# Performance work log

Measured on AMD Instinct MI355X. Metric: run time of the kernel, lower is better.

## Reference

```python
import jax, jax.numpy as jnp
import numpy as np

TEMPERATURE = 0.07
NEG_INF = -1e9  # fp16-safe large negative for masking


def setup_inputs() -> dict:
    key = jax.random.key(0)
    k1, k2 = jax.random.split(key)
    N, D = 4096, 1024
    logits1 = jax.random.normal(k1, (N, D), dtype=jnp.float32)
    logits2 = jax.random.normal(k2, (N, D), dtype=jnp.float32)
    return {"logits1": logits1, "logits2": logits2}


def reference(logits1, logits2):
    # L2-normalize each view along feature dim
    z1 = logits1 / jnp.linalg.norm(logits1, axis=1, keepdims=True)
    z2 = logits2 / jnp.linalg.norm(logits2, axis=1, keepdims=True)
    z = jnp.concatenate([z1, z2], axis=0)  # [2N, D]
    N2 = z.shape[0]
    N = N2 // 2
    sim = jnp.matmul(z, z.T) / TEMPERATURE  # [2N, 2N]
    # positive pair index: i <-> i+N (mod 2N)
    pos_idx = jnp.concatenate([jnp.arange(N) + N, jnp.arange(N)])
    pos_vals = sim[jnp.arange(N2), pos_idx]  # [2N]
    # CE over row = [pos, negs(excl self & pos)] with label 0 is equivalent to
    # -pos + logsumexp over all columns except the diagonal (pos counted once).
    diag_mask = jnp.eye(N2, dtype=bool)
    sim_masked = jnp.where(diag_mask, NEG_INF, sim)
    lse = jax.nn.logsumexp(sim_masked, axis=1)  # [2N]
    loss = jnp.mean(lse - pos_vals)
    return loss
```

## Files before the change

### kernel.cpp

```cpp
#include <hip/hip_runtime.h>
#include <hip/hip_bf16.h>


#define NPAIR 4096
#define NROWS 8192
#define DIM   1024
#define NOFF  496
#define NKT   16
#define INV_T 14.285714285714286f

typedef __attribute__((ext_vector_type(4))) float f32x4;
typedef __attribute__((ext_vector_type(2))) long  i64x2;

#define GLOAD_LDS16(g, l)                                              \
  __builtin_amdgcn_global_load_lds(                                    \
      (const __attribute__((address_space(1))) void*)(g),              \
      (__attribute__((address_space(3))) void*)(l), 16, 0, 0)

#define MFMA_FP8(A, B, C)                                              \
  __builtin_amdgcn_mfma_f32_16x16x32_fp8_fp8((long)(A), (long)(B), (C), 0, 0, 0)

#define WAIT_VM0() asm volatile("s_waitcnt vmcnt(0)" ::: "memory")
#define BARRIER()  { __builtin_amdgcn_s_barrier();                     \
                     __builtin_amdgcn_sched_barrier(0); }

__global__ __launch_bounds__(256) void normalize_kernel(
    const float* __restrict__ l1, const float* __restrict__ l2,
    unsigned char* __restrict__ Z, float* __restrict__ pos,
    float* __restrict__ rowsum) {
  const int i = blockIdx.x;
  const int t = threadIdx.x;
  if (t < 2) rowsum[i * 2 + t] = 0.f;
  const float4 a = ((const float4*)(l1 + (size_t)i * DIM))[t];
  const float4 b = ((const float4*)(l2 + (size_t)i * DIM))[t];
  float s1 = a.x*a.x + a.y*a.y + a.z*a.z + a.w*a.w;
  float s2 = b.x*b.x + b.y*b.y + b.z*b.z + b.w*b.w;
  float d  = a.x*b.x + a.y*b.y + a.z*b.z + a.w*b.w;

  #pragma unroll
  for (int off = 32; off; off >>= 1) {
    s1 += __shfl_down(s1, off);
    s2 += __shfl_down(s2, off);
    d  += __shfl_down(d,  off);
  }
  __shared__ float red[3][4];
  __shared__ float fin[3];
  const int wave = t >> 6, lane = t & 63;
  if (lane == 0) { red[0][wave] = s1; red[1][wave] = s2; red[2][wave] = d; }
  __syncthreads();
  if (t == 0) {
    float S1 = red[0][0] + red[0][1] + red[0][2] + red[0][3];
    float S2 = red[1][0] + red[1][1] + red[1][2] + red[1][3];
    float DD = red[2][0] + red[2][1] + red[2][2] + red[2][3];
    float r1 = rsqrtf(S1), r2 = rsqrtf(S2);
    fin[0] = r1; fin[1] = r2;
    pos[i] = DD * r1 * r2 * INV_T;
  }
  __syncthreads();
  const float r1 = fin[0], r2 = fin[1];
  int pa = __builtin_amdgcn_cvt_pk_fp8_f32(a.x * r1, a.y * r1, 0, false);
  pa     = __builtin_amdgcn_cvt_pk_fp8_f32(a.z * r1, a.w * r1, pa, true);
  int pb = __builtin_amdgcn_cvt_pk_fp8_f32(b.x * r2, b.y * r2, 0, false);
  pb     = __builtin_amdgcn_cvt_pk_fp8_f32(b.z * r2, b.w * r2, pb, true);
  const int k0 = t * 4;
  const int noff = (k0 >> 6) * 64 + (((k0 >> 3) & 3) << 4)
                 + (((k0 >> 5) & 1) << 3) + (k0 & 7);
  *(int*)(Z + (size_t)i * DIM + noff) = pa;
  *(int*)(Z + (size_t)(i + NPAIR) * DIM + noff) = pb;
}

__global__ __launch_bounds__(512, 2) void ntxent_gemm_offdiag(
    const unsigned char* __restrict__ Z, float* __restrict__ rowsum) {
  __shared__ unsigned char lds[3 * 32768];

  const int t    = threadIdx.x;
  const int wid  = t >> 6;
  const int lane = t & 63;
  const int lrow = lane & 15;
  const int kgrp = lane >> 4;
  const int wm   = wid >> 2;
  const int wn   = wid & 3;

  const int idx = (blockIdx.x & 7) * 62 + (blockIdx.x >> 3);
  int bj = (int)((1.0f + sqrtf(1.0f + 8.0f * (float)idx)) * 0.5f);
  while (bj * (bj - 1) / 2 > idx) --bj;
  while ((bj + 1) * bj / 2 <= idx) ++bj;
  const int bi = idx - bj * (bj - 1) / 2;
  const int brow = bi * 256, bcol = bj * 256;

  auto stage_tile = [&](int kt, int bufoff) {
    #pragma unroll
    for (int op = 0; op < 2; ++op) {
      const int rowbase = op ? bcol : brow;
      const int opoff   = op ? 16384 : 0;
      #pragma unroll
      for (int i = 0; i < 2; ++i) {
        const int cb = wid * 128 + i * 64;
        const int c  = cb + lane;
        const int r  = c >> 2;
        const int lc = (c & 3) ^ ((r >> 1) & 3);
        GLOAD_LDS16(Z + (size_t)(rowbase + r) * DIM + kt * 64 + lc * 16,
                    lds + bufoff + opoff + cb * 16);
      }
    }
  };
  auto ld16 = [&](int bufoff, int opoff, int row) -> i64x2 {
    return *(const i64x2*)(lds + bufoff + opoff + row * 64
                           + ((kgrp ^ ((row >> 1) & 3)) << 4));
  };

  i64x2 pa[8], pb[4], qa[8], qb[4];
  f32x4 acc[8][4];
  #pragma unroll
  for (int i = 0; i < 8; ++i)
    #pragma unroll
    for (int j = 0; j < 4; ++j) acc[i][j] = (f32x4){0.f, 0.f, 0.f, 0.f};

#define READF(A_, B_, BO)                                              \
  { _Pragma("unroll") for (int mi = 0; mi < 8; ++mi)                   \
      A_[mi] = ld16((BO), 0, wm * 128 + mi * 16 + lrow);               \
    _Pragma("unroll") for (int ni = 0; ni < 4; ++ni)                   \
      B_[ni] = ld16((BO), 16384, wn * 64 + ni * 16 + lrow); }
#define MMF(A_, B_)                                                    \
  { __builtin_amdgcn_s_setprio(1);                                     \
    _Pragma("unroll") for (int mi = 0; mi < 8; ++mi)                   \
    _Pragma("unroll") for (int ni = 0; ni < 4; ++ni)                   \
      acc[mi][ni] = MFMA_FP8(A_[mi].x, B_[ni].x, acc[mi][ni]);         \
    _Pragma("unroll") for (int mi = 0; mi < 8; ++mi)                   \
    _Pragma("unroll") for (int ni = 0; ni < 4; ++ni)                   \
      acc[mi][ni] = MFMA_FP8(A_[mi].y, B_[ni].y, acc[mi][ni]);         \
    __builtin_amdgcn_s_setprio(0); }

  int oA = 0, oB = 32768, oC = 65536;
  stage_tile(0, oA);
  stage_tile(1, oB);
  WAIT_VM0();
  __syncthreads();
  READF(pa, pb, oA);

  for (int I = 0; I < 8; ++I) {
    const int j = 2 * I;
    WAIT_VM0();
    BARRIER();
    READF(qa, qb, oB);
    if (j + 2 < NKT) stage_tile(j + 2, oC);
    MMF(pa, pb);
    { const int tmp = oA; oA = oB; oB = oC; oC = tmp; }
    WAIT_VM0();
    BARRIER();
    if (j + 2 < NKT) READF(pa, pb, oB);
    if (j + 3 < NKT) stage_tile(j + 3, oC);
    MMF(qa, qb);
    { const int tmp = oA; oA = oB; oB = oC; oC = tmp; }
  }

  #pragma unroll
  for (int mi = 0; mi < 8; ++mi)
    #pragma unroll
    for (int ni = 0; ni < 4; ++ni)
      #pragma unroll
      for (int j = 0; j < 4; ++j)
        acc[mi][ni][j] = __expf((acc[mi][ni][j] - 1.0f) * INV_T);
  #pragma unroll
  for (int mi = 0; mi < 8; ++mi) {
    float rs[4] = {0.f, 0.f, 0.f, 0.f};
    #pragma unroll
    for (int ni = 0; ni < 4; ++ni)
      #pragma unroll
      for (int j = 0; j < 4; ++j) rs[j] += acc[mi][ni][j];
    #pragma unroll
    for (int j = 0; j < 4; ++j) {
      float s = rs[j];
      s += __shfl_xor(s, 1);
      s += __shfl_xor(s, 2);
      s += __shfl_xor(s, 4);
      s += __shfl_xor(s, 8);
      if (lrow == 0)
        atomicAdd(&rowsum[brow + wm * 128 + mi * 16 + kgrp * 4 + j], s);
    }
  }
  #pragma unroll
  for (int ni = 0; ni < 4; ++ni) {
    float cs = 0.f;
    #pragma unroll
    for (int mi = 0; mi < 8; ++mi)
      cs += acc[mi][ni][0] + acc[mi][ni][1] + acc[mi][ni][2] + acc[mi][ni][3];
    cs += __shfl_xor(cs, 16);
    cs += __shfl_xor(cs, 32);
    if (kgrp == 0)
      atomicAdd(&rowsum[bcol + wn * 64 + ni * 16 + lrow], cs);
  }
#undef READF
#undef MMF
}

__global__ __launch_bounds__(512, 2) void ntxent_gemm_diag(
    const unsigned char* __restrict__ Z, float* __restrict__ rowsum) {
  __shared__ unsigned char lds[3 * 24576];

  const int t    = threadIdx.x;
  const int wid  = t >> 6;
  const int lane = t & 63;
  const int lrow = lane & 15;
  const int kgrp = lane >> 4;
  const int wm   = wid >> 2;
  const int wn   = wid & 3;

  const int d = blockIdx.x >> 1;
  const int arow0 = d * 256 + (blockIdx.x & 1) * 128;
  const int bcol0 = d * 256;

  auto stageA = [&](int kt, int buf) {
    const int cb = wid * 64;
    const int c  = cb + lane;
    const int r  = c >> 2;
    const int lc = (c & 3) ^ ((r >> 1) & 3);
    GLOAD_LDS16(Z + (size_t)(arow0 + r) * DIM + kt * 64 + lc * 16,
                lds + buf * 24576 + cb * 16);
  };
  auto stageB = [&](int kt, int buf, int half) {
    const int cb = half * 512 + wid * 64;
    const int c  = cb + lane;
    const int r  = c >> 2;
    const int lc = (c & 3) ^ ((r >> 1) & 3);
    GLOAD_LDS16(Z + (size_t)(bcol0 + r) * DIM + kt * 64 + lc * 16,
                lds + buf * 24576 + 8192 + cb * 16);
  };
  auto ld16 = [&](int buf, int opoff, int row) -> i64x2 {
    return *(const i64x2*)(lds + buf * 24576 + opoff + row * 64
                           + ((kgrp ^ ((row >> 1) & 3)) << 4));
  };

  f32x4 acc[4][4];
  #pragma unroll
  for (int i = 0; i < 4; ++i)
    #pragma unroll
    for (int j = 0; j < 4; ++j) acc[i][j] = (f32x4){0.f, 0.f, 0.f, 0.f};

  stageA(0, 0); stageB(0, 0, 0); stageB(0, 0, 1);
  stageA(1, 1); stageB(1, 1, 0); stageB(1, 1, 1);
  asm volatile("s_waitcnt vmcnt(3)" ::: "memory");
  __builtin_amdgcn_s_barrier();

  int bcur = 0, bnext = 1, bfree = 2;
  for (int kt = 0; kt < NKT; ++kt) {
    i64x2 a[4], b[4];
    #pragma unroll
    for (int mi = 0; mi < 4; ++mi)
      a[mi] = ld16(bcur, 0, wm * 64 + mi * 16 + lrow);
    #pragma unroll
    for (int ni = 0; ni < 4; ++ni)
      b[ni] = ld16(bcur, 8192, wn * 64 + ni * 16 + lrow);
    if (kt + 2 < NKT) {
      stageA(kt + 2, bfree);
      stageB(kt + 2, bfree, 0);
      stageB(kt + 2, bfree, 1);
    }
    asm volatile("s_waitcnt lgkmcnt(0)" ::: "memory");
    __builtin_amdgcn_sched_barrier(0);
    __builtin_amdgcn_s_setprio(1);
    #pragma unroll
    for (int mi = 0; mi < 4; ++mi)
      #pragma unroll
      for (int ni = 0; ni < 4; ++ni)
        acc[mi][ni] = MFMA_FP8(a[mi].x, b[ni].x, acc[mi][ni]);
    #pragma unroll
    for (int mi = 0; mi < 4; ++mi)
      #pragma unroll
      for (int ni = 0; ni < 4; ++ni)
        acc[mi][ni] = MFMA_FP8(a[mi].y, b[ni].y, acc[mi][ni]);
    __builtin_amdgcn_s_setprio(0);
    if (kt + 2 < NKT) {
      asm volatile("s_waitcnt vmcnt(3)" ::: "memory");
    } else if (kt + 1 < NKT) {
      asm volatile("s_waitcnt vmcnt(0)" ::: "memory");
    }
    __builtin_amdgcn_s_barrier();
    const int tmp = bcur; bcur = bnext; bnext = bfree; bfree = tmp;
  }

  #pragma unroll
  for (int mi = 0; mi < 4; ++mi)
    #pragma unroll
    for (int ni = 0; ni < 4; ++ni) {
      const int gcol = bcol0 + wn * 64 + ni * 16 + lrow;
      #pragma unroll
      for (int j = 0; j < 4; ++j) {
        const int grow = arow0 + wm * 64 + mi * 16 + kgrp * 4 + j;
        const float v = acc[mi][ni][j];
        acc[mi][ni][j] = (gcol > grow) ? __expf((v - 1.0f) * INV_T) : 0.f;
      }
    }
  #pragma unroll
  for (int mi = 0; mi < 4; ++mi) {
    float rs[4] = {0.f, 0.f, 0.f, 0.f};
    #pragma unroll
    for (int ni = 0; ni < 4; ++ni)
      #pragma unroll
      for (int j = 0; j < 4; ++j) rs[j] += acc[mi][ni][j];
    #pragma unroll
    for (int j = 0; j < 4; ++j) {
      float s = rs[j];
      s += __shfl_xor(s, 1);
      s += __shfl_xor(s, 2);
      s += __shfl_xor(s, 4);
      s += __shfl_xor(s, 8);
      if (lrow == 0)
        atomicAdd(&rowsum[arow0 + wm * 64 + mi * 16 + kgrp * 4 + j], s);
    }
  }
  #pragma unroll
  for (int ni = 0; ni < 4; ++ni) {
    float cs = 0.f;
    #pragma unroll
    for (int mi = 0; mi < 4; ++mi)
      cs += acc[mi][ni][0] + acc[mi][ni][1] + acc[mi][ni][2] + acc[mi][ni][3];
    cs += __shfl_xor(cs, 16);
    cs += __shfl_xor(cs, 32);
    if (kgrp == 0)
      atomicAdd(&rowsum[bcol0 + wn * 64 + ni * 16 + lrow], cs);
  }
}

__global__ __launch_bounds__(1024) void finalize_kernel(
    const float* __restrict__ rowsum, const float* __restrict__ pos,
    float* __restrict__ out) {
  const int t = threadIdx.x;
  float ls = 0.f, ps = 0.f;
  for (int i = t; i < NROWS; i += 1024) ls += logf(rowsum[i]);
  for (int i = t; i < NPAIR; i += 1024) ps += pos[i];
  #pragma unroll
  for (int off = 32; off; off >>= 1) {
    ls += __shfl_down(ls, off);
    ps += __shfl_down(ps, off);
  }
  __shared__ float sls[16], sps[16];
  const int wave = t >> 6, lane = t & 63;
  if (lane == 0) { sls[wave] = ls; sps[wave] = ps; }
  __syncthreads();
  if (t == 0) {
    float LS = 0.f, PS = 0.f;
    #pragma unroll
    for (int w = 0; w < 16; ++w) { LS += sls[w]; PS += sps[w]; }
    out[0] = INV_T + LS / (float)NROWS - PS / (float)NPAIR;
  }
}

extern "C" void kernel_launch(void* const* d_in, const int* in_sizes, int n_in,
                              void* d_out, int out_size, void* d_ws, size_t ws_size,
                              hipStream_t stream) {
  const float* l1 = (const float*)d_in[0];
  const float* l2 = (const float*)d_in[1];
  float* out = (float*)d_out;

  char* ws = (char*)d_ws;
  unsigned char* Z = (unsigned char*)ws;
  float* rowsum = (float*)(ws + (size_t)NROWS * DIM);
  float* pos    = rowsum + NROWS;

  normalize_kernel<<<NPAIR, 256, 0, stream>>>(l1, l2, Z, pos, rowsum);
  ntxent_gemm_offdiag<<<NOFF, 512, 0, stream>>>(Z, rowsum);
  ntxent_gemm_diag<<<64, 512, 0, stream>>>(Z, rowsum);
  finalize_kernel<<<1, 1024, 0, stream>>>(rowsum, pos, out);
}
```

Measured before the change: 91.89 us.

## Merge diagonal and off-diagonal GEMMs into one launch with deeper LDS pipeline

```diff
diff --git a/kernel.cpp b/kernel.cpp
--- a/kernel.cpp
+++ b/kernel.cpp
@@ -6,6 +6,7 @@
 #define NROWS 8192
 #define DIM   1024
 #define NOFF  496
+#define NTAIL 96
 #define NKT   16
 #define INV_T 14.285714285714286f
 
@@ -20,9 +21,9 @@
 #define MFMA_FP8(A, B, C)                                              \
   __builtin_amdgcn_mfma_f32_16x16x32_fp8_fp8((long)(A), (long)(B), (C), 0, 0, 0)
 
-#define WAIT_VM0() asm volatile("s_waitcnt vmcnt(0)" ::: "memory")
-#define BARRIER()  { __builtin_amdgcn_s_barrier();                     \
-                     __builtin_amdgcn_sched_barrier(0); }
+#define WAIT_VM(N)  asm volatile("s_waitcnt vmcnt(" #N ")" ::: "memory")
+#define BARRIER()   { __builtin_amdgcn_s_barrier();                    \
+                      __builtin_amdgcn_sched_barrier(0); }
 
 __global__ __launch_bounds__(256) void normalize_kernel(
     const float* __restrict__ l1, const float* __restrict__ l2,
@@ -69,52 +70,54 @@
   *(int*)(Z + (size_t)(i + NPAIR) * DIM + noff) = pb;
 }
 
-__global__ __launch_bounds__(512, 2) void ntxent_gemm_offdiag(
+__global__ __launch_bounds__(512, 2) void ntxent_gemm_all(
     const unsigned char* __restrict__ Z, float* __restrict__ rowsum) {
-  __shared__ unsigned char lds[3 * 32768];
+  __shared__ unsigned char lds[131072];
 
   const int t    = threadIdx.x;
   const int wid  = t >> 6;
   const int lane = t & 63;
   const int lrow = lane & 15;
   const int kgrp = lane >> 4;
-  const int wm   = wid >> 2;
-  const int wn   = wid & 3;
-
-  const int idx = (blockIdx.x & 7) * 62 + (blockIdx.x >> 3);
-  int bj = (int)((1.0f + sqrtf(1.0f + 8.0f * (float)idx)) * 0.5f);
-  while (bj * (bj - 1) / 2 > idx) --bj;
-  while ((bj + 1) * bj / 2 <= idx) ++bj;
-  const int bi = idx - bj * (bj - 1) / 2;
-  const int brow = bi * 256, bcol = bj * 256;
-
-  auto stage_tile = [&](int kt, int bufoff) {
-    #pragma unroll
-    for (int op = 0; op < 2; ++op) {
-      const int rowbase = op ? bcol : brow;
-      const int opoff   = op ? 16384 : 0;
-      #pragma unroll
-      for (int i = 0; i < 2; ++i) {
-        const int cb = wid * 128 + i * 64;
-        const int c  = cb + lane;
-        const int r  = c >> 2;
-        const int lc = (c & 3) ^ ((r >> 1) & 3);
-        GLOAD_LDS16(Z + (size_t)(rowbase + r) * DIM + kt * 64 + lc * 16,
-                    lds + bufoff + opoff + cb * 16);
-      }
-    }
-  };
-  auto ld16 = [&](int bufoff, int opoff, int row) -> i64x2 {
-    return *(const i64x2*)(lds + bufoff + opoff + row * 64
-                           + ((kgrp ^ ((row >> 1) & 3)) << 4));
-  };
-
-  i64x2 pa[8], pb[4], qa[8], qb[4];
-  f32x4 acc[8][4];
-  #pragma unroll
-  for (int i = 0; i < 8; ++i)
-    #pragma unroll
-    for (int j = 0; j < 4; ++j) acc[i][j] = (f32x4){0.f, 0.f, 0.f, 0.f};
+
+  if (blockIdx.x < NOFF) {
+    const int wm = wid >> 2;
+    const int wn = wid & 3;
+
+    const int idx = (blockIdx.x & 7) * 62 + (blockIdx.x >> 3);
+    int bj = (int)((1.0f + sqrtf(1.0f + 8.0f * (float)idx)) * 0.5f);
+    while (bj * (bj - 1) / 2 > idx) --bj;
+    while ((bj + 1) * bj / 2 <= idx) ++bj;
+    const int bi = idx - bj * (bj - 1) / 2;
+    const int brow = bi * 256, bcol = bj * 256;
+
+    auto stage_tile = [&](int kt, int bufoff) {
+      #pragma unroll
+      for (int op = 0; op < 2; ++op) {
+        const int rowbase = op ? bcol : brow;
+        const int opoff   = op ? 16384 : 0;
+        #pragma unroll
+        for (int i = 0; i < 2; ++i) {
+          const int cb = wid * 128 + i * 64;
+          const int c  = cb + lane;
+          const int r  = c >> 2;
+          const int lc = (c & 3) ^ ((r >> 1) & 3);
+          GLOAD_LDS16(Z + (size_t)(rowbase + r) * DIM + kt * 64 + lc * 16,
+                      lds + bufoff + opoff + cb * 16);
+        }
+      }
+    };
+    auto ld16 = [&](int bufoff, int opoff, int row) -> i64x2 {
+      return *(const i64x2*)(lds + bufoff + opoff + row * 64
+                             + ((kgrp ^ ((row >> 1) & 3)) << 4));
+    };
+
+    i64x2 pa[8], pb[4], qa[8], qb[4];
+    f32x4 acc[8][4];
+    #pragma unroll
+    for (int i = 0; i < 8; ++i)
+      #pragma unroll
+      for (int j = 0; j < 4; ++j) acc[i][j] = (f32x4){0.f, 0.f, 0.f, 0.f};
 
 #define READF(A_, B_, BO)                                              \
   { _Pragma("unroll") for (int mi = 0; mi < 8; ++mi)                   \
@@ -131,194 +134,171 @@
       acc[mi][ni] = MFMA_FP8(A_[mi].y, B_[ni].y, acc[mi][ni]);         \
     __builtin_amdgcn_s_setprio(0); }
 
-  int oA = 0, oB = 32768, oC = 65536;
-  stage_tile(0, oA);
-  stage_tile(1, oB);
-  WAIT_VM0();
-  __syncthreads();
-  READF(pa, pb, oA);
-
-  for (int I = 0; I < 8; ++I) {
-    const int j = 2 * I;
-    WAIT_VM0();
-    BARRIER();
-    READF(qa, qb, oB);
-    if (j + 2 < NKT) stage_tile(j + 2, oC);
-    MMF(pa, pb);
-    { const int tmp = oA; oA = oB; oB = oC; oC = tmp; }
-    WAIT_VM0();
-    BARRIER();
-    if (j + 2 < NKT) READF(pa, pb, oB);
-    if (j + 3 < NKT) stage_tile(j + 3, oC);
-    MMF(qa, qb);
-    { const int tmp = oA; oA = oB; oB = oC; oC = tmp; }
-  }
-
-  #pragma unroll
-  for (int mi = 0; mi < 8; ++mi)
-    #pragma unroll
-    for (int ni = 0; ni < 4; ++ni)
-      #pragma unroll
-      for (int j = 0; j < 4; ++j)
-        acc[mi][ni][j] = __expf((acc[mi][ni][j] - 1.0f) * INV_T);
-  #pragma unroll
-  for (int mi = 0; mi < 8; ++mi) {
-    float rs[4] = {0.f, 0.f, 0.f, 0.f};
-    #pragma unroll
-    for (int ni = 0; ni < 4; ++ni)
-      #pragma unroll
-      for (int j = 0; j < 4; ++j) rs[j] += acc[mi][ni][j];
-    #pragma unroll
-    for (int j = 0; j < 4; ++j) {
-      float s = rs[j];
-      s += __shfl_xor(s, 1);
-      s += __shfl_xor(s, 2);
-      s += __shfl_xor(s, 4);
-      s += __shfl_xor(s, 8);
-      if (lrow == 0)
-        atomicAdd(&rowsum[brow + wm * 128 + mi * 16 + kgrp * 4 + j], s);
-    }
-  }
-  #pragma unroll
-  for (int ni = 0; ni < 4; ++ni) {
-    float cs = 0.f;
-    #pragma unroll
-    for (int mi = 0; mi < 8; ++mi)
-      cs += acc[mi][ni][0] + acc[mi][ni][1] + acc[mi][ni][2] + acc[mi][ni][3];
-    cs += __shfl_xor(cs, 16);
-    cs += __shfl_xor(cs, 32);
-    if (kgrp == 0)
-      atomicAdd(&rowsum[bcol + wn * 64 + ni * 16 + lrow], cs);
-  }
+    stage_tile(0, 0);
+    stage_tile(1, 32768);
+    stage_tile(2, 65536);
+    WAIT_VM(8);
+    __syncthreads();
+    READF(pa, pb, 0);
+
+    #pragma unroll
+    for (int h = 0; h < NKT; ++h) {
+      const int bo_next  = ((h + 1) & 3) * 32768;
+      const int bo_stage = ((h + 3) & 3) * 32768;
+      if (h <= NKT - 3) { WAIT_VM(4); } else { WAIT_VM(0); }
+      BARRIER();
+      if (h + 1 < NKT) {
+        if (h & 1) { READF(pa, pb, bo_next); }
+        else       { READF(qa, qb, bo_next); }
+      }
+      if (h + 3 < NKT) stage_tile(h + 3, bo_stage);
+      if (h & 1) { MMF(qa, qb); } else { MMF(pa, pb); }
+    }
 #undef READF
 #undef MMF
-}
-
-__global__ __launch_bounds__(512, 2) void ntxent_gemm_diag(
-    const unsigned char* __restrict__ Z, float* __restrict__ rowsum) {
-  __shared__ unsigned char lds[3 * 24576];
-
-  const int t    = threadIdx.x;
-  const int wid  = t >> 6;
-  const int lane = t & 63;
-  const int lrow = lane & 15;
-  const int kgrp = lane >> 4;
-  const int wm   = wid >> 2;
-  const int wn   = wid & 3;
-
-  const int d = blockIdx.x >> 1;
-  const int arow0 = d * 256 + (blockIdx.x & 1) * 128;
-  const int bcol0 = d * 256;
-
-  auto stageA = [&](int kt, int buf) {
-    const int cb = wid * 64;
-    const int c  = cb + lane;
-    const int r  = c >> 2;
-    const int lc = (c & 3) ^ ((r >> 1) & 3);
-    GLOAD_LDS16(Z + (size_t)(arow0 + r) * DIM + kt * 64 + lc * 16,
-                lds + buf * 24576 + cb * 16);
-  };
-  auto stageB = [&](int kt, int buf, int half) {
-    const int cb = half * 512 + wid * 64;
-    const int c  = cb + lane;
-    const int r  = c >> 2;
-    const int lc = (c & 3) ^ ((r >> 1) & 3);
-    GLOAD_LDS16(Z + (size_t)(bcol0 + r) * DIM + kt * 64 + lc * 16,
-                lds + buf * 24576 + 8192 + cb * 16);
-  };
-  auto ld16 = [&](int buf, int opoff, int row) -> i64x2 {
-    return *(const i64x2*)(lds + buf * 24576 + opoff + row * 64
-                           + ((kgrp ^ ((row >> 1) & 3)) << 4));
-  };
-
-  f32x4 acc[4][4];
-  #pragma unroll
-  for (int i = 0; i < 4; ++i)
-    #pragma unroll
-    for (int j = 0; j < 4; ++j) acc[i][j] = (f32x4){0.f, 0.f, 0.f, 0.f};
-
-  stageA(0, 0); stageB(0, 0, 0); stageB(0, 0, 1);
-  stageA(1, 1); stageB(1, 1, 0); stageB(1, 1, 1);
-  asm volatile("s_waitcnt vmcnt(3)" ::: "memory");
-  __builtin_amdgcn_s_barrier();
-
-  int bcur = 0, bnext = 1, bfree = 2;
-  for (int kt = 0; kt < NKT; ++kt) {
-    i64x2 a[4], b[4];
+
+    #pragma unroll
+    for (int mi = 0; mi < 8; ++mi)
+      #pragma unroll
+      for (int ni = 0; ni < 4; ++ni)
+        #pragma unroll
+        for (int j = 0; j < 4; ++j)
+          acc[mi][ni][j] = __expf((acc[mi][ni][j] - 1.0f) * INV_T);
+    #pragma unroll
+    for (int mi = 0; mi < 8; ++mi) {
+      float rs[4] = {0.f, 0.f, 0.f, 0.f};
+      #pragma unroll
+      for (int ni = 0; ni < 4; ++ni)
+        #pragma unroll
+        for (int j = 0; j < 4; ++j) rs[j] += acc[mi][ni][j];
+      #pragma unroll
+      for (int j = 0; j < 4; ++j) {
+        float s = rs[j];
+        s += __shfl_xor(s, 1);
+        s += __shfl_xor(s, 2);
+        s += __shfl_xor(s, 4);
+        s += __shfl_xor(s, 8);
+        if (lrow == 0)
+          atomicAdd(&rowsum[brow + wm * 128 + mi * 16 + kgrp * 4 + j], s);
+      }
+    }
+    #pragma unroll
+    for (int ni = 0; ni < 4; ++ni) {
+      float cs = 0.f;
+      #pragma unroll
+      for (int mi = 0; mi < 8; ++mi)
+        cs += acc[mi][ni][0] + acc[mi][ni][1] + acc[mi][ni][2] + acc[mi][ni][3];
+      cs += __shfl_xor(cs, 16);
+      cs += __shfl_xor(cs, 32);
+      if (kgrp == 0)
+        atomicAdd(&rowsum[bcol + wn * 64 + ni * 16 + lrow], cs);
+    }
+  } else {
+    const int b2 = blockIdx.x - NOFF;
+    const int d  = b2 / 3, ty = b2 - d * 3;
+    const int arow0 = d * 256 + (ty == 2 ? 128 : 0);
+    const int bcol0 = d * 256 + (ty >= 1 ? 128 : 0);
+    const int wm = wid >> 2;
+    const int wn = wid & 3;
+
+    auto stage = [&](int kt, int buf, int rowbase, int opoff) {
+      const int cb = wid * 64;
+      const int c  = cb + lane;
+      const int r  = c >> 2;
+      const int lc = (c & 3) ^ ((r >> 1) & 3);
+      GLOAD_LDS16(Z + (size_t)(rowbase + r) * DIM + kt * 64 + lc * 16,
+                  lds + buf * 16384 + opoff + cb * 16);
+    };
+    auto ld16 = [&](int buf, int opoff, int row) -> i64x2 {
+      return *(const i64x2*)(lds + buf * 16384 + opoff + row * 64
+                             + ((kgrp ^ ((row >> 1) & 3)) << 4));
+    };
+
+    f32x4 acc[4][2];
+    #pragma unroll
+    for (int i = 0; i < 4; ++i)
+      #pragma unroll
+      for (int j = 0; j < 2; ++j) acc[i][j] = (f32x4){0.f, 0.f, 0.f, 0.f};
+
+    stage(0, 0, arow0, 0); stage(0, 0, bcol0, 8192);
+    stage(1, 1, arow0, 0); stage(1, 1, bcol0, 8192);
+    WAIT_VM(2);
+    __builtin_amdgcn_s_barrier();
+
+    int bcur = 0, bnext = 1, bfree = 2;
+    for (int kt = 0; kt < NKT; ++kt) {
+      i64x2 a[4], b[2];
+      #pragma unroll
+      for (int mi = 0; mi < 4; ++mi)
+        a[mi] = ld16(bcur, 0, wm * 64 + mi * 16 + lrow);
+      #pragma unroll
+      for (int ni = 0; ni < 2; ++ni)
+        b[ni] = ld16(bcur, 8192, wn * 32 + ni * 16 + lrow);
+      if (kt + 2 < NKT) {
+        stage(kt + 2, bfree, arow0, 0);
+        stage(kt + 2, bfree, bcol0, 8192);
+      }
+      asm volatile("s_waitcnt lgkmcnt(0)" ::: "memory");
+      __builtin_amdgcn_sched_barrier(0);
+      __builtin_amdgcn_s_setprio(1);
+      #pragma unroll
+      for (int mi = 0; mi < 4; ++mi)
+        #pragma unroll
+        for (int ni = 0; ni < 2; ++ni)
+          acc[mi][ni] = MFMA_FP8(a[mi].x, b[ni].x, acc[mi][ni]);
+      #pragma unroll
+      for (int mi = 0; mi < 4; ++mi)
+        #pragma unroll
+        for (int ni = 0; ni < 2; ++ni)
+          acc[mi][ni] = MFMA_FP8(a[mi].y, b[ni].y, acc[mi][ni]);
+      __builtin_amdgcn_s_setprio(0);
+      if (kt + 2 < NKT) { WAIT_VM(2); }
+      else if (kt + 1 < NKT) { WAIT_VM(0); }
+      __builtin_amdgcn_s_barrier();
+      const int tmp = bcur; bcur = bnext; bnext = bfree; bfree = tmp;
+    }
+
     #pragma unroll
     for (int mi = 0; mi < 4; ++mi)
-      a[mi] = ld16(bcur, 0, wm * 64 + mi * 16 + lrow);
-    #pragma unroll
-    for (int ni = 0; ni < 4; ++ni)
-      b[ni] = ld16(bcur, 8192, wn * 64 + ni * 16 + lrow);
-    if (kt + 2 < NKT) {
-      stageA(kt + 2, bfree);
-      stageB(kt + 2, bfree, 0);
-      stageB(kt + 2, bfree, 1);
-    }
-    asm volatile("s_waitcnt lgkmcnt(0)" ::: "memory");
-    __builtin_amdgcn_sched_barrier(0);
-    __builtin_amdgcn_s_setprio(1);
-    #pragma unroll
-    for (int mi = 0; mi < 4; ++mi)
-      #pragma unroll
-      for (int ni = 0; ni < 4; ++ni)
-        acc[mi][ni] = MFMA_FP8(a[mi].x, b[ni].x, acc[mi][ni]);
-    #pragma unroll
-    for (int mi = 0; mi < 4; ++mi)
-      #pragma unroll
-      for (int ni = 0; ni < 4; ++ni)
-        acc[mi][ni] = MFMA_FP8(a[mi].y, b[ni].y, acc[mi][ni]);
-    __builtin_amdgcn_s_setprio(0);
-    if (kt + 2 < NKT) {
-      asm volatile("s_waitcnt vmcnt(3)" ::: "memory");
-    } else if (kt + 1 < NKT) {
-      asm volatile("s_waitcnt vmcnt(0)" ::: "memory");
-    }
-    __builtin_amdgcn_s_barrier();
-    const int tmp = bcur; bcur = bnext; bnext = bfree; bfree = tmp;
-  }
-
-  #pragma unroll
-  for (int mi = 0; mi < 4; ++mi)
-    #pragma unroll
-    for (int ni = 0; ni < 4; ++ni) {
-      const int gcol = bcol0 + wn * 64 + ni * 16 + lrow;
+      #pragma unroll
+      for (int ni = 0; ni < 2; ++ni) {
+        const int gcol = bcol0 + wn * 32 + ni * 16 + lrow;
+        #pragma unroll
+        for (int j = 0; j < 4; ++j) {
+          const int grow = arow0 + wm * 64 + mi * 16 + kgrp * 4 + j;
+          const float v = acc[mi][ni][j];
+          acc[mi][ni][j] = (gcol > grow) ? __expf((v - 1.0f) * INV_T) : 0.f;
+        }
+      }
+    #pragma unroll
+    for (int mi = 0; mi < 4; ++mi) {
+      float rs[4] = {0.f, 0.f, 0.f, 0.f};
+      #pragma unroll
+      for (int ni = 0; ni < 2; ++ni)
+        #pragma unroll
+        for (int j = 0; j < 4; ++j) rs[j] += acc[mi][ni][j];
       #pragma unroll
       for (int j = 0; j < 4; ++j) {
-        const int grow = arow0 + wm * 64 + mi * 16 + kgrp * 4 + j;
-        const float v = acc[mi][ni][j];
-        acc[mi][ni][j] = (gcol > grow) ? __expf((v - 1.0f) * INV_T) : 0.f;
-      }
-    }
-  #pragma unroll
-  for (int mi = 0; mi < 4; ++mi) {
-    float rs[4] = {0.f, 0.f, 0.f, 0.f};
-    #pragma unroll
-    for (int ni = 0; ni < 4; ++ni)
-      #pragma unroll
-      for (int j = 0; j < 4; ++j) rs[j] += acc[mi][ni][j];
-    #pragma unroll
-    for (int j = 0; j < 4; ++j) {
-      float s = rs[j];
-      s += __shfl_xor(s, 1);
-      s += __shfl_xor(s, 2);
-      s += __shfl_xor(s, 4);
-      s += __shfl_xor(s, 8);
-      if (lrow == 0)
-        atomicAdd(&rowsum[arow0 + wm * 64 + mi * 16 + kgrp * 4 + j], s);
-    }
-  }
-  #pragma unroll
-  for (int ni = 0; ni < 4; ++ni) {
-    float cs = 0.f;
-    #pragma unroll
-    for (int mi = 0; mi < 4; ++mi)
-      cs += acc[mi][ni][0] + acc[mi][ni][1] + acc[mi][ni][2] + acc[mi][ni][3];
-    cs += __shfl_xor(cs, 16);
-    cs += __shfl_xor(cs, 32);
-    if (kgrp == 0)
-      atomicAdd(&rowsum[bcol0 + wn * 64 + ni * 16 + lrow], cs);
+        float s = rs[j];
+        s += __shfl_xor(s, 1);
+        s += __shfl_xor(s, 2);
+        s += __shfl_xor(s, 4);
+        s += __shfl_xor(s, 8);
+        if (lrow == 0)
+          atomicAdd(&rowsum[arow0 + wm * 64 + mi * 16 + kgrp * 4 + j], s);
+      }
+    }
+    #pragma unroll
+    for (int ni = 0; ni < 2; ++ni) {
+      float cs = 0.f;
+      #pragma unroll
+      for (int mi = 0; mi < 4; ++mi)
+        cs += acc[mi][ni][0] + acc[mi][ni][1] + acc[mi][ni][2] + acc[mi][ni][3];
+      cs += __shfl_xor(cs, 16);
+      cs += __shfl_xor(cs, 32);
+      if (kgrp == 0)
+        atomicAdd(&rowsum[bcol0 + wn * 32 + ni * 16 + lrow], cs);
+    }
   }
 }
 
@@ -359,7 +339,6 @@
   float* pos    = rowsum + NROWS;
 
   normalize_kernel<<<NPAIR, 256, 0, stream>>>(l1, l2, Z, pos, rowsum);
-  ntxent_gemm_offdiag<<<NOFF, 512, 0, stream>>>(Z, rowsum);
-  ntxent_gemm_diag<<<64, 512, 0, stream>>>(Z, rowsum);
+  ntxent_gemm_all<<<NOFF + NTAIL, 512, 0, stream>>>(Z, rowsum);
   finalize_kernel<<<1, 1024, 0, stream>>>(rowsum, pos, out);
 }
```

After: 91.05 us. No clear change (-0.9%).
